# Kernel optimization log

Hardware: AMD Instinct MI355X
Metric: run time of the kernel (lower is better)

The kernel has to match this reference:

```python
import jax, jax.numpy as jnp
import numpy as np

NUM_EXPERTS = 8
TOP_K = 2
HIDDEN = 1024
INTER = 2048
TOKENS = 2048


def setup_inputs() -> dict:
    key = jax.random.key(0)
    k1, k2, k3, k4, k5 = jax.random.split(key, 5)
    inputs = jax.random.normal(k1, (TOKENS, HIDDEN), dtype=jnp.float32)
    router_logits = jax.random.normal(k2, (TOKENS, NUM_EXPERTS), dtype=jnp.float32)
    # expert weights, normal init (as nnx.initializers.normal -> stddev 0.01-ish; use 0.02)
    wi_0 = jax.random.normal(k3, (NUM_EXPERTS, HIDDEN, INTER), dtype=jnp.float32) * 0.02
    wi_1 = jax.random.normal(k4, (NUM_EXPERTS, HIDDEN, INTER), dtype=jnp.float32) * 0.02
    wo = jax.random.normal(k5, (NUM_EXPERTS, INTER, HIDDEN), dtype=jnp.float32) * 0.02
    return {"inputs": inputs, "router_logits": router_logits,
            "wi_0": wi_0, "wi_1": wi_1, "wo": wo}


def reference(inputs, router_logits, wi_0, wi_1, wo):
    T, H = inputs.shape
    E = wi_0.shape[0]
    K = TOP_K

    # --- routing: top-k + softmax over top-k logits (+ redundant renorm, as in source) ---
    top_k_logits, top_k_indices = jax.lax.top_k(router_logits, K)  # [T,K]
    w = jax.nn.softmax(top_k_logits, axis=-1)
    w = w / jnp.sum(w, axis=-1, keepdims=True)                      # [T,K]

    # --- permute: replicate each token K times, sort token-expert pairs by expert ---
    flat_experts = top_k_indices.reshape(-1)                        # [T*K], token-major
    sort_idx = jnp.argsort(flat_experts)                            # stable sort
    x_rep = jnp.repeat(inputs, K, axis=0)                           # [T*K, H]
    x_sorted = x_rep[sort_idx]                                      # rows grouped by expert
    group_sizes = jnp.bincount(flat_experts, length=E).astype(jnp.int32)  # [E]

    # --- grouped GEMM (ragged over contiguous expert groups): SwiGLU expert MLP ---
    h0 = jax.lax.ragged_dot(x_sorted, wi_0, group_sizes)            # [T*K, INTER]
    h1 = jax.lax.ragged_dot(x_sorted, wi_1, group_sizes)            # [T*K, INTER]
    inter = jax.nn.silu(h0) * h1
    y = jax.lax.ragged_dot(inter, wo, group_sizes)                  # [T*K, H]

    # --- unpermute + weighted combine ---
    y_unperm = jnp.zeros_like(y).at[sort_idx].set(y)                # back to token-major
    out = jnp.einsum('tkh,tk->th', y_unperm.reshape(T, K, H), w)
    return out
```

## Files before the change

### kernel.cpp

```cpp
#include <hip/hip_runtime.h>
#include <hip/hip_bf16.h>

#define T_TOKENS 2048
#define NE 8
#define HID 1024
#define INTER_ 2048
#define NPAIR (T_TOKENS * 2)

typedef unsigned short u16;
typedef __attribute__((ext_vector_type(4))) float f32x4;
typedef __attribute__((ext_vector_type(8))) short s16x8;

__device__ __forceinline__ u16 f2b(float f) {
    union { float f; unsigned u; } v; v.f = f;
    unsigned r = v.u + 0x7fffu + ((v.u >> 16) & 1u);
    return (u16)(r >> 16);
}

__device__ __forceinline__ void gl_lds16(const u16* g, u16* l) {
    __builtin_amdgcn_global_load_lds(
        (const __attribute__((address_space(1))) unsigned int*)g,
        (__attribute__((address_space(3))) unsigned int*)l, 16, 0, 0);
}

__global__ void route_kernel(const float* __restrict__ logits,
                             int* cnt, int* tokE, float* tokW) {
    int t = blockIdx.x * 256 + threadIdx.x;
    if (t >= T_TOKENS) return;
    float l[NE];
#pragma unroll
    for (int i = 0; i < NE; i++) l[i] = logits[t * NE + i];
    int i0 = 0; float m0 = l[0];
#pragma unroll
    for (int i = 1; i < NE; i++) if (l[i] > m0) { m0 = l[i]; i0 = i; }
    int i1 = -1; float m1 = -1e30f;
#pragma unroll
    for (int i = 0; i < NE; i++) if (i != i0 && l[i] > m1) { m1 = l[i]; i1 = i; }
    float w0 = 1.f / (1.f + expf(m1 - m0));
    tokE[2 * t] = i0; tokE[2 * t + 1] = i1;
    tokW[2 * t] = w0; tokW[2 * t + 1] = 1.f - w0;
    atomicAdd(&cnt[i0], 1);
    atomicAdd(&cnt[i1], 1);
}

__global__ void scan_kernel(const int* __restrict__ cnt, int* offs, int* cursor) {
    if (threadIdx.x == 0 && blockIdx.x == 0) {
        int a = 0;
        for (int e = 0; e < NE; e++) { offs[e] = a; cursor[e] = a; a += cnt[e]; }
        offs[NE] = a;
    }
}

__global__ void scatter_kernel(const int* __restrict__ tokE, int* cursor,
                               int* pair_tok, int* pair_slot) {
    int t = blockIdx.x * 256 + threadIdx.x;
    if (t >= T_TOKENS) return;
#pragma unroll
    for (int k = 0; k < 2; k++) {
        int e = tokE[2 * t + k];
        int slot = atomicAdd(&cursor[e], 1);
        pair_tok[slot] = t;
        pair_slot[2 * t + k] = slot;
    }
}

__global__ void cvt_x_kernel(const float* __restrict__ x, u16* __restrict__ xb) {
    int i = blockIdx.x * 256 + threadIdx.x;
    float4 v = ((const float4*)x)[i];
    ushort4 b;
    b.x = f2b(v.x); b.y = f2b(v.y); b.z = f2b(v.z); b.w = f2b(v.w);
    ((ushort4*)xb)[i] = b;
}

__global__ __launch_bounds__(256) void transpose_kernel(const float* __restrict__ W,
                                                        u16* __restrict__ Wt,
                                                        int K, int N) {
    int e = blockIdx.z;
    const float* Win = W + (size_t)e * K * N;
    u16* Wout = Wt + (size_t)e * N * K;
    int nb = blockIdx.x * 64, kb = blockIdx.y * 64;
    __shared__ __align__(16) u16 tile[64 * 68];
    int tid = threadIdx.x;
#pragma unroll
    for (int p = 0; p < 4; p++) {
        int c = tid + p * 256;
        int r = c >> 4, c4 = c & 15;
        float4 v = *(const float4*)&Win[(size_t)(kb + r) * N + nb + c4 * 4];
        ushort4 b;
        b.x = f2b(v.x); b.y = f2b(v.y); b.z = f2b(v.z); b.w = f2b(v.w);
        *(ushort4*)&tile[r * 68 + c4 * 4] = b;
    }
    __syncthreads();
#pragma unroll
    for (int p = 0; p < 2; p++) {
        int k8 = p * 4 + (tid >> 6);
        int n = tid & 63;
        __align__(16) u16 tmp[8];
#pragma unroll
        for (int j = 0; j < 8; j++) tmp[j] = tile[(k8 * 8 + j) * 68 + n];
        *(uint4*)&Wout[(size_t)(nb + n) * K + kb + k8 * 8] = *(const uint4*)tmp;
    }
}

__global__ __launch_bounds__(256, 2) void fused_up_kernel(
        const u16* __restrict__ A, const u16* __restrict__ B0t, const u16* __restrict__ B1t,
        const int* __restrict__ pair_tok, const int* __restrict__ offs,
        u16* __restrict__ intr) {
    int e = blockIdx.z;
    int off = offs[e];
    int cnt = offs[e + 1] - off;
    int row0 = blockIdx.y * 128;
    if (row0 >= cnt) return;
    int nt = blockIdx.x * 128;

    __shared__ __align__(16) u16 As[128 * 32];
    __shared__ __align__(16) u16 Bs0[128 * 32];
    __shared__ __align__(16) u16 Bs1[128 * 32];

    int tid = threadIdx.x;
    int wave = tid >> 6, lane = tid & 63;

    const u16* gA[2]; const u16* gB0[2]; const u16* gB1[2];
    u16 *lA[2], *lB0[2], *lB1[2];
    const size_t eNK = (size_t)e * INTER_ * HID;
#pragma unroll
    for (int h = 0; h < 2; h++) {
        int c = 2 * wave + h;
        int r = c * 16 + (lane >> 2);
        int seg = lane & 3;
        int mr = row0 + r; if (mr > cnt - 1) mr = cnt - 1;
        int arow = pair_tok[off + mr];
        gA[h]  = A + (size_t)arow * HID + seg * 8;
        gB0[h] = B0t + eNK + (size_t)(nt + r) * HID + seg * 8;
        gB1[h] = B1t + eNK + (size_t)(nt + r) * HID + seg * 8;
        lA[h]  = As  + c * 512;
        lB0[h] = Bs0 + c * 512;
        lB1[h] = Bs1 + c * 512;
    }

    int wr = (wave >> 1) * 64, wc = (wave & 1) * 64;
    int fm = lane & 15, fk = (lane >> 4) * 8;

    f32x4 acc0[4][4], acc1[4][4];
#pragma unroll
    for (int i = 0; i < 4; i++)
#pragma unroll
        for (int j = 0; j < 4; j++) {
            acc0[i][j] = (f32x4){0.f, 0.f, 0.f, 0.f};
            acc1[i][j] = (f32x4){0.f, 0.f, 0.f, 0.f};
        }

    for (int kb = 0; kb < HID; kb += 32) {
#pragma unroll
        for (int h = 0; h < 2; h++) {
            gl_lds16(gA[h] + kb, lA[h]);
            gl_lds16(gB0[h] + kb, lB0[h]);
            gl_lds16(gB1[h] + kb, lB1[h]);
        }
        __syncthreads();
        s16x8 af[4];
#pragma unroll
        for (int i = 0; i < 4; i++)
            af[i] = *(const s16x8*)&As[(wr + i * 16 + fm) * 32 + fk];
#pragma unroll
        for (int j = 0; j < 4; j++) {
            s16x8 b0 = *(const s16x8*)&Bs0[(wc + j * 16 + fm) * 32 + fk];
            s16x8 b1 = *(const s16x8*)&Bs1[(wc + j * 16 + fm) * 32 + fk];
#pragma unroll
            for (int i = 0; i < 4; i++) {
                acc0[i][j] = __builtin_amdgcn_mfma_f32_16x16x32_bf16(af[i], b0, acc0[i][j], 0, 0, 0);
                acc1[i][j] = __builtin_amdgcn_mfma_f32_16x16x32_bf16(af[i], b1, acc1[i][j], 0, 0, 0);
            }
        }
        __syncthreads();
    }

    int r4 = (lane >> 4) * 4, cc = lane & 15;
#pragma unroll
    for (int i = 0; i < 4; i++) {
#pragma unroll
        for (int reg = 0; reg < 4; reg++) {
            int rr = wr + i * 16 + r4 + reg;
            if (row0 + rr < cnt) {
                size_t slot = (size_t)(off + row0 + rr);
#pragma unroll
                for (int j = 0; j < 4; j++) {
                    int col = nt + wc + j * 16 + cc;
                    float a = acc0[i][j][reg];
                    float b = acc1[i][j][reg];
                    float s = a / (1.f + __expf(-a)) * b;
                    intr[slot * INTER_ + col] = f2b(s);
                }
            }
        }
    }
}

__global__ __launch_bounds__(256, 2) void down_kernel(
        const u16* __restrict__ A, const u16* __restrict__ Bt,
        const int* __restrict__ offs, float* __restrict__ ypart) {
    int e = blockIdx.z >> 1, ks = blockIdx.z & 1;
    int off = offs[e];
    int cnt = offs[e + 1] - off;
    int row0 = blockIdx.y * 128;
    if (row0 >= cnt) return;
    int nt = blockIdx.x * 128;

    __shared__ __align__(16) u16 As[128 * 32];
    __shared__ __align__(16) u16 Bs[128 * 32];

    int tid = threadIdx.x;
    int wave = tid >> 6, lane = tid & 63;

    const u16* gA[2]; const u16* gB[2];
    u16 *lA[2], *lB[2];
    const size_t eNK = (size_t)e * HID * INTER_;
#pragma unroll
    for (int h = 0; h < 2; h++) {
        int c = 2 * wave + h;
        int r = c * 16 + (lane >> 2);
        int seg = lane & 3;
        int mr = row0 + r; if (mr > cnt - 1) mr = cnt - 1;
        gA[h] = A + (size_t)(off + mr) * INTER_ + seg * 8;
        gB[h] = Bt + eNK + (size_t)(nt + r) * INTER_ + seg * 8;
        lA[h] = As + c * 512;
        lB[h] = Bs + c * 512;
    }

    int wr = (wave >> 1) * 64, wc = (wave & 1) * 64;
    int fm = lane & 15, fk = (lane >> 4) * 8;

    f32x4 acc[4][4];
#pragma unroll
    for (int i = 0; i < 4; i++)
#pragma unroll
        for (int j = 0; j < 4; j++) acc[i][j] = (f32x4){0.f, 0.f, 0.f, 0.f};

    int kend = ks * 1024 + 1024;
    for (int kb = ks * 1024; kb < kend; kb += 32) {
#pragma unroll
        for (int h = 0; h < 2; h++) {
            gl_lds16(gA[h] + kb, lA[h]);
            gl_lds16(gB[h] + kb, lB[h]);
        }
        __syncthreads();
        s16x8 af[4], bfr[4];
#pragma unroll
        for (int i = 0; i < 4; i++)
            af[i] = *(const s16x8*)&As[(wr + i * 16 + fm) * 32 + fk];
#pragma unroll
        for (int j = 0; j < 4; j++)
            bfr[j] = *(const s16x8*)&Bs[(wc + j * 16 + fm) * 32 + fk];
#pragma unroll
        for (int i = 0; i < 4; i++)
#pragma unroll
            for (int j = 0; j < 4; j++)
                acc[i][j] = __builtin_amdgcn_mfma_f32_16x16x32_bf16(af[i], bfr[j], acc[i][j], 0, 0, 0);
        __syncthreads();
    }

    int r4 = (lane >> 4) * 4, cc = lane & 15;
    float* yout = ypart + (size_t)ks * NPAIR * HID;
#pragma unroll
    for (int i = 0; i < 4; i++) {
#pragma unroll
        for (int reg = 0; reg < 4; reg++) {
            int rr = wr + i * 16 + r4 + reg;
            if (row0 + rr < cnt) {
                size_t slot = (size_t)(off + row0 + rr);
#pragma unroll
                for (int j = 0; j < 4; j++) {
                    int col = nt + wc + j * 16 + cc;
                    yout[slot * HID + col] = acc[i][j][reg];
                }
            }
        }
    }
}

__global__ void combine_kernel(const float* __restrict__ y0, const float* __restrict__ y1,
                               const int* __restrict__ pair_slot,
                               const float* __restrict__ tokW, float* __restrict__ out) {
    int i = blockIdx.x * 256 + threadIdx.x;
    int t = i >> 8;
    int h4 = i & 255;
    int s0 = pair_slot[2 * t], s1 = pair_slot[2 * t + 1];
    float w0 = tokW[2 * t], w1 = tokW[2 * t + 1];
    float4 a0 = ((const float4*)y0)[(size_t)s0 * 256 + h4];
    float4 a1 = ((const float4*)y1)[(size_t)s0 * 256 + h4];
    float4 b0 = ((const float4*)y0)[(size_t)s1 * 256 + h4];
    float4 b1 = ((const float4*)y1)[(size_t)s1 * 256 + h4];
    float4 r;
    r.x = w0 * (a0.x + a1.x) + w1 * (b0.x + b1.x);
    r.y = w0 * (a0.y + a1.y) + w1 * (b0.y + b1.y);
    r.z = w0 * (a0.z + a1.z) + w1 * (b0.z + b1.z);
    r.w = w0 * (a0.w + a1.w) + w1 * (b0.w + b1.w);
    ((float4*)out)[i] = r;
}

extern "C" void kernel_launch(void* const* d_in, const int* in_sizes, int n_in,
                              void* d_out, int out_size, void* d_ws, size_t ws_size,
                              hipStream_t stream) {
    (void)in_sizes; (void)n_in; (void)out_size; (void)ws_size;
    const float* x   = (const float*)d_in[0];
    const float* rl  = (const float*)d_in[1];
    const float* wi0 = (const float*)d_in[2];
    const float* wi1 = (const float*)d_in[3];
    const float* wo  = (const float*)d_in[4];
    float* out = (float*)d_out;

    char* p = (char*)d_ws;
    auto alloc = [&](size_t bytes) -> void* {
        void* r = (void*)p;
        p += (bytes + 255) & ~(size_t)255;
        return r;
    };
    u16* xb   = (u16*)alloc((size_t)T_TOKENS * HID * 2);
    u16* wt0  = (u16*)alloc((size_t)NE * HID * INTER_ * 2);
    u16* wt1  = (u16*)alloc((size_t)NE * HID * INTER_ * 2);
    u16* wto  = (u16*)alloc((size_t)NE * HID * INTER_ * 2);
    u16* intr = (u16*)alloc((size_t)NPAIR * INTER_ * 2);
    float* ypart = (float*)alloc((size_t)2 * NPAIR * HID * 4);
    int* cnt      = (int*)alloc(NE * sizeof(int));
    int* offs     = (int*)alloc((NE + 1) * sizeof(int));
    int* cursor   = (int*)alloc(NE * sizeof(int));
    int* tokE     = (int*)alloc(NPAIR * sizeof(int));
    float* tokW   = (float*)alloc(NPAIR * sizeof(float));
    int* pair_tok = (int*)alloc(NPAIR * sizeof(int));
    int* pair_slot= (int*)alloc(NPAIR * sizeof(int));

    hipMemsetAsync(cnt, 0, NE * sizeof(int), stream);
    route_kernel<<<T_TOKENS / 256, 256, 0, stream>>>(rl, cnt, tokE, tokW);
    scan_kernel<<<1, 64, 0, stream>>>(cnt, offs, cursor);
    scatter_kernel<<<T_TOKENS / 256, 256, 0, stream>>>(tokE, cursor, pair_tok, pair_slot);
    cvt_x_kernel<<<T_TOKENS * HID / 4 / 256, 256, 0, stream>>>(x, xb);

    dim3 tgi(INTER_ / 64, HID / 64, NE);
    transpose_kernel<<<tgi, 256, 0, stream>>>(wi0, wt0, HID, INTER_);
    transpose_kernel<<<tgi, 256, 0, stream>>>(wi1, wt1, HID, INTER_);
    dim3 tgo(HID / 64, INTER_ / 64, NE);
    transpose_kernel<<<tgo, 256, 0, stream>>>(wo, wto, INTER_, HID);

    dim3 g1(INTER_ / 128, 16, NE);
    fused_up_kernel<<<g1, 256, 0, stream>>>(xb, wt0, wt1, pair_tok, offs, intr);
    dim3 g2(HID / 128, 16, NE * 2);
    down_kernel<<<g2, 256, 0, stream>>>(intr, wto, offs, ypart);
    combine_kernel<<<T_TOKENS * HID / 4 / 256, 256, 0, stream>>>(
        ypart, ypart + (size_t)NPAIR * HID, pair_slot, tokW, out);
}
```

Before: 391.3 us.

## Fuse routing and transposes, widen GEMM K-tile with swizzle, atomic combine

Routing, scan and scatter become one single-block kernel using shared-memory counters. The three weight transposes become one launch. Both grouped GEMMs now load 64-wide K tiles into an XOR-swizzled LDS layout to halve barrier count and avoid bank conflicts. The down GEMM scales its output by the routing weight and atomically adds into a zeroed output, removing the partial buffer and the combine kernel. The cost is fp32 atomic traffic and a serial single-block routing step.

Measured after the change: 349.2 us. -10.8%, faster.

```diff
diff --git a/kernel.cpp b/kernel.cpp
--- a/kernel.cpp
+++ b/kernel.cpp
@@ -23,44 +23,47 @@
         (__attribute__((address_space(3))) unsigned int*)l, 16, 0, 0);
 }
 
-__global__ void route_kernel(const float* __restrict__ logits,
-                             int* cnt, int* tokE, float* tokW) {
-    int t = blockIdx.x * 256 + threadIdx.x;
-    if (t >= T_TOKENS) return;
-    float l[NE];
-#pragma unroll
-    for (int i = 0; i < NE; i++) l[i] = logits[t * NE + i];
-    int i0 = 0; float m0 = l[0];
-#pragma unroll
-    for (int i = 1; i < NE; i++) if (l[i] > m0) { m0 = l[i]; i0 = i; }
-    int i1 = -1; float m1 = -1e30f;
-#pragma unroll
-    for (int i = 0; i < NE; i++) if (i != i0 && l[i] > m1) { m1 = l[i]; i1 = i; }
-    float w0 = 1.f / (1.f + expf(m1 - m0));
-    tokE[2 * t] = i0; tokE[2 * t + 1] = i1;
-    tokW[2 * t] = w0; tokW[2 * t + 1] = 1.f - w0;
-    atomicAdd(&cnt[i0], 1);
-    atomicAdd(&cnt[i1], 1);
-}
-
-__global__ void scan_kernel(const int* __restrict__ cnt, int* offs, int* cursor) {
-    if (threadIdx.x == 0 && blockIdx.x == 0) {
+__global__ __launch_bounds__(256) void route_all(const float* __restrict__ logits,
+                                                 int* __restrict__ offs,
+                                                 int* __restrict__ pair_tok,
+                                                 float* __restrict__ pair_w) {
+    __shared__ int s_cnt[NE];
+    __shared__ int s_cur[NE];
+    __shared__ short s_e0[T_TOKENS];
+    __shared__ short s_e1[T_TOKENS];
+    __shared__ float s_w0[T_TOKENS];
+    int tid = threadIdx.x;
+    if (tid < NE) s_cnt[tid] = 0;
+    __syncthreads();
+    for (int t = tid; t < T_TOKENS; t += 256) {
+        float l[NE];
+#pragma unroll
+        for (int i = 0; i < NE; i++) l[i] = logits[t * NE + i];
+        int i0 = 0; float m0 = l[0];
+#pragma unroll
+        for (int i = 1; i < NE; i++) if (l[i] > m0) { m0 = l[i]; i0 = i; }
+        int i1 = -1; float m1 = -1e30f;
+#pragma unroll
+        for (int i = 0; i < NE; i++) if (i != i0 && l[i] > m1) { m1 = l[i]; i1 = i; }
+        float w0 = 1.f / (1.f + __expf(m1 - m0));
+        s_e0[t] = (short)i0; s_e1[t] = (short)i1; s_w0[t] = w0;
+        atomicAdd(&s_cnt[i0], 1);
+        atomicAdd(&s_cnt[i1], 1);
+    }
+    __syncthreads();
+    if (tid == 0) {
         int a = 0;
-        for (int e = 0; e < NE; e++) { offs[e] = a; cursor[e] = a; a += cnt[e]; }
+        for (int e = 0; e < NE; e++) { offs[e] = a; s_cur[e] = a; a += s_cnt[e]; }
         offs[NE] = a;
     }
-}
-
-__global__ void scatter_kernel(const int* __restrict__ tokE, int* cursor,
-                               int* pair_tok, int* pair_slot) {
-    int t = blockIdx.x * 256 + threadIdx.x;
-    if (t >= T_TOKENS) return;
-#pragma unroll
-    for (int k = 0; k < 2; k++) {
-        int e = tokE[2 * t + k];
-        int slot = atomicAdd(&cursor[e], 1);
-        pair_tok[slot] = t;
-        pair_slot[2 * t + k] = slot;
+    __syncthreads();
+    for (int t = tid; t < T_TOKENS; t += 256) {
+        int i0 = s_e0[t], i1 = s_e1[t];
+        float w0 = s_w0[t];
+        int sl0 = atomicAdd(&s_cur[i0], 1);
+        pair_tok[sl0] = t; pair_w[sl0] = w0;
+        int sl1 = atomicAdd(&s_cur[i1], 1);
+        pair_tok[sl1] = t; pair_w[sl1] = 1.f - w0;
     }
 }
 
@@ -72,13 +75,22 @@
     ((ushort4*)xb)[i] = b;
 }
 
-__global__ __launch_bounds__(256) void transpose_kernel(const float* __restrict__ W,
-                                                        u16* __restrict__ Wt,
-                                                        int K, int N) {
-    int e = blockIdx.z;
+__global__ __launch_bounds__(256) void transpose_all(const float* __restrict__ wi0,
+                                                     const float* __restrict__ wi1,
+                                                     const float* __restrict__ wo,
+                                                     u16* __restrict__ wt0,
+                                                     u16* __restrict__ wt1,
+                                                     u16* __restrict__ wto) {
+    int wsel = blockIdx.y >> 3, e = blockIdx.y & 7;
+    const float* W; u16* Wt; int K, N, nb, kb;
+    int bx = blockIdx.x;
+    if (wsel == 0)      { W = wi0; Wt = wt0; }
+    else if (wsel == 1) { W = wi1; Wt = wt1; }
+    else                { W = wo;  Wt = wto; }
+    if (wsel < 2) { K = HID; N = INTER_; nb = (bx & 31) * 64; kb = (bx >> 5) * 64; }
+    else          { K = INTER_; N = HID; nb = (bx & 15) * 64; kb = (bx >> 4) * 64; }
     const float* Win = W + (size_t)e * K * N;
     u16* Wout = Wt + (size_t)e * N * K;
-    int nb = blockIdx.x * 64, kb = blockIdx.y * 64;
     __shared__ __align__(16) u16 tile[64 * 68];
     int tid = threadIdx.x;
 #pragma unroll
@@ -113,33 +125,33 @@
     if (row0 >= cnt) return;
     int nt = blockIdx.x * 128;
 
-    __shared__ __align__(16) u16 As[128 * 32];
-    __shared__ __align__(16) u16 Bs0[128 * 32];
-    __shared__ __align__(16) u16 Bs1[128 * 32];
+    __shared__ __align__(16) u16 As[128 * 64];
+    __shared__ __align__(16) u16 Bs0[128 * 64];
+    __shared__ __align__(16) u16 Bs1[128 * 64];
 
     int tid = threadIdx.x;
     int wave = tid >> 6, lane = tid & 63;
 
-    const u16* gA[2]; const u16* gB0[2]; const u16* gB1[2];
-    u16 *lA[2], *lB0[2], *lB1[2];
+    const u16 *gA[4], *gB0[4], *gB1[4];
+    u16 *lA[4], *lB0[4], *lB1[4];
     const size_t eNK = (size_t)e * INTER_ * HID;
 #pragma unroll
-    for (int h = 0; h < 2; h++) {
-        int c = 2 * wave + h;
-        int r = c * 16 + (lane >> 2);
-        int seg = lane & 3;
+    for (int is = 0; is < 4; is++) {
+        int c = wave * 4 + is;
+        int r = c * 8 + (lane >> 3);
+        int sg = (lane & 7) ^ (r & 7);
         int mr = row0 + r; if (mr > cnt - 1) mr = cnt - 1;
         int arow = pair_tok[off + mr];
-        gA[h]  = A + (size_t)arow * HID + seg * 8;
-        gB0[h] = B0t + eNK + (size_t)(nt + r) * HID + seg * 8;
-        gB1[h] = B1t + eNK + (size_t)(nt + r) * HID + seg * 8;
-        lA[h]  = As  + c * 512;
-        lB0[h] = Bs0 + c * 512;
-        lB1[h] = Bs1 + c * 512;
+        gA[is]  = A + (size_t)arow * HID + sg * 8;
+        gB0[is] = B0t + eNK + (size_t)(nt + r) * HID + sg * 8;
+        gB1[is] = B1t + eNK + (size_t)(nt + r) * HID + sg * 8;
+        lA[is]  = As  + c * 512;
+        lB0[is] = Bs0 + c * 512;
+        lB1[is] = Bs1 + c * 512;
     }
 
     int wr = (wave >> 1) * 64, wc = (wave & 1) * 64;
-    int fm = lane & 15, fk = (lane >> 4) * 8;
+    int fm = lane & 15, quad = lane >> 4;
 
     f32x4 acc0[4][4], acc1[4][4];
 #pragma unroll
@@ -150,32 +162,39 @@
             acc1[i][j] = (f32x4){0.f, 0.f, 0.f, 0.f};
         }
 
-    for (int kb = 0; kb < HID; kb += 32) {
-#pragma unroll
-        for (int h = 0; h < 2; h++) {
-            gl_lds16(gA[h] + kb, lA[h]);
-            gl_lds16(gB0[h] + kb, lB0[h]);
-            gl_lds16(gB1[h] + kb, lB1[h]);
+    for (int kb = 0; kb < HID; kb += 64) {
+#pragma unroll
+        for (int is = 0; is < 4; is++) {
+            gl_lds16(gA[is] + kb, lA[is]);
+            gl_lds16(gB0[is] + kb, lB0[is]);
+            gl_lds16(gB1[is] + kb, lB1[is]);
         }
         __syncthreads();
-        s16x8 af[4];
-#pragma unroll
-        for (int i = 0; i < 4; i++)
-            af[i] = *(const s16x8*)&As[(wr + i * 16 + fm) * 32 + fk];
-#pragma unroll
-        for (int j = 0; j < 4; j++) {
-            s16x8 b0 = *(const s16x8*)&Bs0[(wc + j * 16 + fm) * 32 + fk];
-            s16x8 b1 = *(const s16x8*)&Bs1[(wc + j * 16 + fm) * 32 + fk];
+#pragma unroll
+        for (int step = 0; step < 2; step++) {
+            int f = step * 4 + quad;
+            s16x8 af[4];
 #pragma unroll
             for (int i = 0; i < 4; i++) {
-                acc0[i][j] = __builtin_amdgcn_mfma_f32_16x16x32_bf16(af[i], b0, acc0[i][j], 0, 0, 0);
-                acc1[i][j] = __builtin_amdgcn_mfma_f32_16x16x32_bf16(af[i], b1, acc1[i][j], 0, 0, 0);
+                int R = wr + i * 16 + fm;
+                af[i] = *(const s16x8*)&As[R * 64 + ((f ^ (R & 7)) * 8)];
+            }
+#pragma unroll
+            for (int j = 0; j < 4; j++) {
+                int R = wc + j * 16 + fm;
+                s16x8 b0 = *(const s16x8*)&Bs0[R * 64 + ((f ^ (R & 7)) * 8)];
+                s16x8 b1 = *(const s16x8*)&Bs1[R * 64 + ((f ^ (R & 7)) * 8)];
+#pragma unroll
+                for (int i = 0; i < 4; i++) {
+                    acc0[i][j] = __builtin_amdgcn_mfma_f32_16x16x32_bf16(af[i], b0, acc0[i][j], 0, 0, 0);
+                    acc1[i][j] = __builtin_amdgcn_mfma_f32_16x16x32_bf16(af[i], b1, acc1[i][j], 0, 0, 0);
+                }
             }
         }
         __syncthreads();
     }
 
-    int r4 = (lane >> 4) * 4, cc = lane & 15;
+    int r4 = quad * 4, cc = lane & 15;
 #pragma unroll
     for (int i = 0; i < 4; i++) {
 #pragma unroll
@@ -198,7 +217,8 @@
 
 __global__ __launch_bounds__(256, 2) void down_kernel(
         const u16* __restrict__ A, const u16* __restrict__ Bt,
-        const int* __restrict__ offs, float* __restrict__ ypart) {
+        const int* __restrict__ offs, const int* __restrict__ pair_tok,
+        const float* __restrict__ pair_w, float* __restrict__ out) {
     int e = blockIdx.z >> 1, ks = blockIdx.z & 1;
     int off = offs[e];
     int cnt = offs[e + 1] - off;
@@ -206,29 +226,29 @@
     if (row0 >= cnt) return;
     int nt = blockIdx.x * 128;
 
-    __shared__ __align__(16) u16 As[128 * 32];
-    __shared__ __align__(16) u16 Bs[128 * 32];
+    __shared__ __align__(16) u16 As[128 * 64];
+    __shared__ __align__(16) u16 Bs[128 * 64];
 
     int tid = threadIdx.x;
     int wave = tid >> 6, lane = tid & 63;
 
-    const u16* gA[2]; const u16* gB[2];
-    u16 *lA[2], *lB[2];
+    const u16 *gA[4], *gB[4];
+    u16 *lA[4], *lB[4];
     const size_t eNK = (size_t)e * HID * INTER_;
 #pragma unroll
-    for (int h = 0; h < 2; h++) {
-        int c = 2 * wave + h;
-        int r = c * 16 + (lane >> 2);
-        int seg = lane & 3;
+    for (int is = 0; is < 4; is++) {
+        int c = wave * 4 + is;
+        int r = c * 8 + (lane >> 3);
+        int sg = (lane & 7) ^ (r & 7);
         int mr = row0 + r; if (mr > cnt - 1) mr = cnt - 1;
-        gA[h] = A + (size_t)(off + mr) * INTER_ + seg * 8;
-        gB[h] = Bt + eNK + (size_t)(nt + r) * INTER_ + seg * 8;
-        lA[h] = As + c * 512;
-        lB[h] = Bs + c * 512;
+        gA[is] = A + (size_t)(off + mr) * INTER_ + sg * 8;
+        gB[is] = Bt + eNK + (size_t)(nt + r) * INTER_ + sg * 8;
+        lA[is] = As + c * 512;
+        lB[is] = Bs + c * 512;
     }
 
     int wr = (wave >> 1) * 64, wc = (wave & 1) * 64;
-    int fm = lane & 15, fk = (lane >> 4) * 8;
+    int fm = lane & 15, quad = lane >> 4;
 
     f32x4 acc[4][4];
 #pragma unroll
@@ -237,71 +257,60 @@
         for (int j = 0; j < 4; j++) acc[i][j] = (f32x4){0.f, 0.f, 0.f, 0.f};
 
     int kend = ks * 1024 + 1024;
-    for (int kb = ks * 1024; kb < kend; kb += 32) {
-#pragma unroll
-        for (int h = 0; h < 2; h++) {
-            gl_lds16(gA[h] + kb, lA[h]);
-            gl_lds16(gB[h] + kb, lB[h]);
+    for (int kb = ks * 1024; kb < kend; kb += 64) {
+#pragma unroll
+        for (int is = 0; is < 4; is++) {
+            gl_lds16(gA[is] + kb, lA[is]);
+            gl_lds16(gB[is] + kb, lB[is]);
         }
         __syncthreads();
-        s16x8 af[4], bfr[4];
-#pragma unroll
-        for (int i = 0; i < 4; i++)
-            af[i] = *(const s16x8*)&As[(wr + i * 16 + fm) * 32 + fk];
-#pragma unroll
-        for (int j = 0; j < 4; j++)
-            bfr[j] = *(const s16x8*)&Bs[(wc + j * 16 + fm) * 32 + fk];
-#pragma unroll
-        for (int i = 0; i < 4; i++)
-#pragma unroll
-            for (int j = 0; j < 4; j++)
-                acc[i][j] = __builtin_amdgcn_mfma_f32_16x16x32_bf16(af[i], bfr[j], acc[i][j], 0, 0, 0);
+#pragma unroll
+        for (int step = 0; step < 2; step++) {
+            int f = step * 4 + quad;
+            s16x8 af[4], bfr[4];
+#pragma unroll
+            for (int i = 0; i < 4; i++) {
+                int R = wr + i * 16 + fm;
+                af[i] = *(const s16x8*)&As[R * 64 + ((f ^ (R & 7)) * 8)];
+            }
+#pragma unroll
+            for (int j = 0; j < 4; j++) {
+                int R = wc + j * 16 + fm;
+                bfr[j] = *(const s16x8*)&Bs[R * 64 + ((f ^ (R & 7)) * 8)];
+            }
+#pragma unroll
+            for (int i = 0; i < 4; i++)
+#pragma unroll
+                for (int j = 0; j < 4; j++)
+                    acc[i][j] = __builtin_amdgcn_mfma_f32_16x16x32_bf16(af[i], bfr[j], acc[i][j], 0, 0, 0);
+        }
         __syncthreads();
     }
 
-    int r4 = (lane >> 4) * 4, cc = lane & 15;
-    float* yout = ypart + (size_t)ks * NPAIR * HID;
+    int r4 = quad * 4, cc = lane & 15;
 #pragma unroll
     for (int i = 0; i < 4; i++) {
 #pragma unroll
         for (int reg = 0; reg < 4; reg++) {
             int rr = wr + i * 16 + r4 + reg;
             if (row0 + rr < cnt) {
-                size_t slot = (size_t)(off + row0 + rr);
+                int slot = off + row0 + rr;
+                int t = pair_tok[slot];
+                float w = pair_w[slot];
 #pragma unroll
                 for (int j = 0; j < 4; j++) {
                     int col = nt + wc + j * 16 + cc;
-                    yout[slot * HID + col] = acc[i][j][reg];
+                    atomicAdd(&out[(size_t)t * HID + col], w * acc[i][j][reg]);
                 }
             }
         }
     }
-}
-
-__global__ void combine_kernel(const float* __restrict__ y0, const float* __restrict__ y1,
-                               const int* __restrict__ pair_slot,
-                               const float* __restrict__ tokW, float* __restrict__ out) {
-    int i = blockIdx.x * 256 + threadIdx.x;
-    int t = i >> 8;
-    int h4 = i & 255;
-    int s0 = pair_slot[2 * t], s1 = pair_slot[2 * t + 1];
-    float w0 = tokW[2 * t], w1 = tokW[2 * t + 1];
-    float4 a0 = ((const float4*)y0)[(size_t)s0 * 256 + h4];
-    float4 a1 = ((const float4*)y1)[(size_t)s0 * 256 + h4];
-    float4 b0 = ((const float4*)y0)[(size_t)s1 * 256 + h4];
-    float4 b1 = ((const float4*)y1)[(size_t)s1 * 256 + h4];
-    float4 r;
-    r.x = w0 * (a0.x + a1.x) + w1 * (b0.x + b1.x);
-    r.y = w0 * (a0.y + a1.y) + w1 * (b0.y + b1.y);
-    r.z = w0 * (a0.z + a1.z) + w1 * (b0.z + b1.z);
-    r.w = w0 * (a0.w + a1.w) + w1 * (b0.w + b1.w);
-    ((float4*)out)[i] = r;
 }
 
 extern "C" void kernel_launch(void* const* d_in, const int* in_sizes, int n_in,
                               void* d_out, int out_size, void* d_ws, size_t ws_size,
                               hipStream_t stream) {
-    (void)in_sizes; (void)n_in; (void)out_size; (void)ws_size;
+    (void)in_sizes; (void)n_in; (void)ws_size;
     const float* x   = (const float*)d_in[0];
     const float* rl  = (const float*)d_in[1];
     const float* wi0 = (const float*)d_in[2];
@@ -320,31 +329,17 @@
     u16* wt1  = (u16*)alloc((size_t)NE * HID * INTER_ * 2);
     u16* wto  = (u16*)alloc((size_t)NE * HID * INTER_ * 2);
     u16* intr = (u16*)alloc((size_t)NPAIR * INTER_ * 2);
-    float* ypart = (float*)alloc((size_t)2 * NPAIR * HID * 4);
-    int* cnt      = (int*)alloc(NE * sizeof(int));
     int* offs     = (int*)alloc((NE + 1) * sizeof(int));
-    int* cursor   = (int*)alloc(NE * sizeof(int));
-    int* tokE     = (int*)alloc(NPAIR * sizeof(int));
-    float* tokW   = (float*)alloc(NPAIR * sizeof(float));
     int* pair_tok = (int*)alloc(NPAIR * sizeof(int));
-    int* pair_slot= (int*)alloc(NPAIR * sizeof(int));
-
-    hipMemsetAsync(cnt, 0, NE * sizeof(int), stream);
-    route_kernel<<<T_TOKENS / 256, 256, 0, stream>>>(rl, cnt, tokE, tokW);
-    scan_kernel<<<1, 64, 0, stream>>>(cnt, offs, cursor);
-    scatter_kernel<<<T_TOKENS / 256, 256, 0, stream>>>(tokE, cursor, pair_tok, pair_slot);
+    float* pair_w = (float*)alloc(NPAIR * sizeof(float));
+
+    hipMemsetAsync(out, 0, (size_t)out_size * sizeof(float), stream);
+    route_all<<<1, 256, 0, stream>>>(rl, offs, pair_tok, pair_w);
     cvt_x_kernel<<<T_TOKENS * HID / 4 / 256, 256, 0, stream>>>(x, xb);
-
-    dim3 tgi(INTER_ / 64, HID / 64, NE);
-    transpose_kernel<<<tgi, 256, 0, stream>>>(wi0, wt0, HID, INTER_);
-    transpose_kernel<<<tgi, 256, 0, stream>>>(wi1, wt1, HID, INTER_);
-    dim3 tgo(HID / 64, INTER_ / 64, NE);
-    transpose_kernel<<<tgo, 256, 0, stream>>>(wo, wto, INTER_, HID);
+    transpose_all<<<dim3(512, 24), 256, 0, stream>>>(wi0, wi1, wo, wt0, wt1, wto);
 
     dim3 g1(INTER_ / 128, 16, NE);
     fused_up_kernel<<<g1, 256, 0, stream>>>(xb, wt0, wt1, pair_tok, offs, intr);
     dim3 g2(HID / 128, 16, NE * 2);
-    down_kernel<<<g2, 256, 0, stream>>>(intr, wto, offs, ypart);
-    combine_kernel<<<T_TOKENS * HID / 4 / 256, 256, 0, stream>>>(
-        ypart, ypart + (size_t)NPAIR * HID, pair_slot, tokW, out);
-}
+    down_kernel<<<g2, 256, 0, stream>>>(intr, wto, offs, pair_tok, pair_w, out);
+}
```
